# Kernel tuning notes

Hardware: AMD Instinct MI355X
Metric: run time of the kernel (lower is better)

## Reference

```python
import jax, jax.numpy as jnp
import numpy as np

B, T, N, H = 256, 512, 128, 128  # batch, timesteps(l), num_classes, num_hidden


def setup_inputs() -> dict:
    key = jax.random.key(0)
    ks = jax.random.split(key, 7)
    s = 0.05
    return {
        "x": jax.random.normal(ks[0], (B, T, N), dtype=jnp.float32),
        "Wf": jax.random.normal(ks[1], (N, 4 * H), dtype=jnp.float32) * s,
        "Uf": jax.random.normal(ks[2], (H, 4 * H), dtype=jnp.float32) * s,
        "bf": jax.random.normal(ks[3], (4 * H,), dtype=jnp.float32) * s,
        "Wb": jax.random.normal(ks[4], (N, 4 * H), dtype=jnp.float32) * s,
        "Ub": jax.random.normal(ks[5], (H, 4 * H), dtype=jnp.float32) * s,
        "bb": jax.random.normal(ks[6], (4 * H,), dtype=jnp.float32) * s,
    }


def _lstm_scan(xs, W, U, b):
    # xs: [T, B, N]; Keras gate order i, f, g(c), o. Zero initial state.
    def step(carry, xt):
        h, c = carry
        z = xt @ W + h @ U + b  # [B, 4H]
        i, f, g, o = jnp.split(z, 4, axis=-1)
        i = jax.nn.sigmoid(i)
        f = jax.nn.sigmoid(f)
        g = jnp.tanh(g)
        o = jax.nn.sigmoid(o)
        c = f * c + i * g
        h = o * jnp.tanh(c)
        return (h, c), h

    h0 = jnp.zeros((xs.shape[1], U.shape[0]), dtype=xs.dtype)
    c0 = jnp.zeros_like(h0)
    _, hs = jax.lax.scan(step, (h0, c0), xs)
    return hs  # [T, B, H]


def reference(x, Wf, Uf, bf, Wb, Ub, bb):
    xs = jnp.transpose(x, (1, 0, 2))  # [T, B, N]
    f_hs = _lstm_scan(xs, Wf, Uf, bf)            # forward over t = 0..T-1
    b_hs = _lstm_scan(xs[::-1], Wb, Ub, bb)      # backward cell over reversed seq
    # Original code stacks concat(f_h_i, b_h_i) at loop index i WITHOUT
    # re-reversing the backward stream, so we concat step-aligned streams.
    out = jnp.concatenate([f_hs, b_hs], axis=-1)  # [T, B, 2H]
    return jnp.transpose(out, (1, 0, 2))  # [B, T, 2H]
```

## Files before the change

### kernel.cpp

```cpp
#include <hip/hip_runtime.h>


typedef short s16x8 __attribute__((ext_vector_type(8)));
typedef float f32x4 __attribute__((ext_vector_type(4)));

#define NT 512
#define LDSROW 264

#define LDS_BARRIER() asm volatile("s_waitcnt lgkmcnt(0)\n\ts_barrier" ::: "memory")

__device__ __forceinline__ unsigned short f2bf(float f) {
  unsigned int u = __float_as_uint(f);
  u += 0x7fffu + ((u >> 16) & 1u);
  return (unsigned short)(u >> 16);
}
__device__ __forceinline__ float sigm(float x) {
  return __builtin_amdgcn_rcpf(1.f + __expf(-x));
}
__device__ __forceinline__ float tanh_(float x) {
  float xc = fminf(fmaxf(x, -12.f), 12.f);
  return 1.f - 2.f * __builtin_amdgcn_rcpf(1.f + __expf(2.f * xc));
}

__global__ void prep_frags(const float* __restrict__ Wf, const float* __restrict__ Uf,
                           const float* __restrict__ Wb, const float* __restrict__ Ub,
                           unsigned short* __restrict__ frag) {
  int idx = blockIdx.x * 256 + threadIdx.x;
  int j    = idx & 7;
  int lane = (idx >> 3) & 63;
  int tile = (idx >> 9) & 7;
  int kc   = (idx >> 12) & 7;
  int gate = (idx >> 15) & 3;
  int dir  = (idx >> 17) & 1;
  const float* M = (kc < 4) ? (dir ? Wb : Wf) : (dir ? Ub : Uf);
  int k   = (kc & 3) * 32 + (lane >> 4) * 8 + j;
  int col = gate * 128 + tile * 16 + (lane & 15);
  frag[idx] = f2bf(M[k * 512 + col]);
}

__global__ __launch_bounds__(512, 2) void bilstm_rec(
    const unsigned short* __restrict__ frag, const float* __restrict__ x,
    const float* __restrict__ bfw, const float* __restrict__ bbw,
    float* __restrict__ out) {
  __shared__ unsigned short xh[2][16][LDSROW];

  int bid = blockIdx.x;
  int bblk = bid & 63, dir = bid >> 6;
  int tid = threadIdx.x;
  int tc = tid >> 6, lane = tid & 63, quad = lane >> 4, m = lane & 15;
  bool mrow = ((m & 3) == 0);

  s16x8 wu[4][8];
#pragma unroll
  for (int g = 0; g < 4; g++)
#pragma unroll
    for (int kc = 0; kc < 8; kc++)
      wu[g][kc] = *(const s16x8*)(frag +
          ((((size_t)(dir * 4 + g) * 8 + kc) * 8 + tc) * 64 + lane) * 8);

  const float* bias = dir ? bbw : bfw;
  float bv[4];
#pragma unroll
  for (int g = 0; g < 4; g++) bv[g] = bias[g * 128 + tc * 16 + m];

  int srow = tid >> 7, scol = tid & 127;
  const float* xsrc = x + ((size_t)(bblk * 4 + srow) * NT) * 128 + scol;

  auto tmap = [&](int s) { int ss = s > NT - 1 ? NT - 1 : s; return dir ? (NT - 1 - ss) : ss; };

  {
    unsigned int* zp = (unsigned int*)&xh[0][0][0];
    for (int i = tid; i < 2 * 16 * (LDSROW / 2); i += 512) zp[i] = 0;
  }

  float vxA = xsrc[(size_t)tmap(2) * 128];
  float vxB = xsrc[(size_t)tmap(3) * 128];

  float vx1 = xsrc[(size_t)tmap(1) * 128];
  float vx0 = xsrc[(size_t)tmap(0) * 128];
  xh[0][srow * 4][scol] = f2bf(vx1);
  xh[1][srow * 4][scol] = f2bf(vx0);
  __syncthreads();

  s16x8 ah[4], ax[4];
#pragma unroll
  for (int kk = 0; kk < 4; kk++) { ah[kk] = (s16x8){0,0,0,0,0,0,0,0}; ax[kk] = (s16x8){0,0,0,0,0,0,0,0}; }

  if (mrow) {
#pragma unroll
    for (int kk = 0; kk < 4; kk++)
      ax[kk] = *(const s16x8*)(&xh[1][m][kk * 32 + quad * 8]);
  }
  __syncthreads();

  f32x4 accA[4], accB[4];
#pragma unroll
  for (int g = 0; g < 4; g++) {
    accA[g][0] = bv[g]; accA[g][1] = bv[g]; accA[g][2] = bv[g]; accA[g][3] = bv[g];
  }
#pragma unroll
  for (int kk = 0; kk < 4; kk++)
#pragma unroll
    for (int g = 0; g < 4; g++)
      accA[g] = __builtin_amdgcn_mfma_f32_16x16x32_bf16(ax[kk], wu[g][kk], accA[g], 0, 0, 0);

  float cc = 0.f;
  float* outp = out + ((size_t)(bblk * 4 + quad) * NT) * 256 + dir * 128 + tc * 16 + m;

  auto body = [&](int s, float& vx, f32x4 (&accC)[4], f32x4 (&accN)[4]) {
    int cb = s & 1, nb = cb ^ 1;

    float vnew = xsrc[(size_t)tmap(s + 4) * 128];

    if (mrow) {
#pragma unroll
      for (int kk = 0; kk < 4; kk++)
        ah[kk] = *(const s16x8*)(&xh[cb][m][128 + kk * 32 + quad * 8]);
#pragma unroll
      for (int kk = 0; kk < 4; kk++)
        ax[kk] = *(const s16x8*)(&xh[cb][m][kk * 32 + quad * 8]);
    }

#pragma unroll
    for (int kk = 0; kk < 4; kk++)
#pragma unroll
      for (int g = 0; g < 4; g++)
        accC[g] = __builtin_amdgcn_mfma_f32_16x16x32_bf16(ah[kk], wu[g][4 + kk], accC[g], 0, 0, 0);

#pragma unroll
    for (int g = 0; g < 4; g++) {
      accN[g][0] = bv[g]; accN[g][1] = bv[g]; accN[g][2] = bv[g]; accN[g][3] = bv[g];
    }
#pragma unroll
    for (int kk = 0; kk < 4; kk++)
#pragma unroll
      for (int g = 0; g < 4; g++)
        accN[g] = __builtin_amdgcn_mfma_f32_16x16x32_bf16(ax[kk], wu[g][kk], accN[g], 0, 0, 0);

    float iv = sigm(accC[0][0]);
    float fv = sigm(accC[1][0]);
    float gv = tanh_(accC[2][0]);
    float ov = sigm(accC[3][0]);
    cc = fv * cc + iv * gv;
    float hv = ov * tanh_(cc);

    xh[nb][quad * 4][128 + tc * 16 + m] = f2bf(hv);
    xh[nb][srow * 4][scol] = f2bf(vx);

    outp[(size_t)s * 256] = hv;

    LDS_BARRIER();
    vx = vnew;
  };

  for (int s = 0; s < NT; s += 2) {
    body(s, vxA, accA, accB);
    body(s + 1, vxB, accB, accA);
  }
}

extern "C" void kernel_launch(void* const* d_in, const int* in_sizes, int n_in,
                              void* d_out, int out_size, void* d_ws, size_t ws_size,
                              hipStream_t stream) {
  const float* x  = (const float*)d_in[0];
  const float* Wf = (const float*)d_in[1];
  const float* Uf = (const float*)d_in[2];
  const float* bf = (const float*)d_in[3];
  const float* Wb = (const float*)d_in[4];
  const float* Ub = (const float*)d_in[5];
  const float* bb = (const float*)d_in[6];
  float* out = (float*)d_out;

  unsigned short* frag = (unsigned short*)d_ws;

  prep_frags<<<1024, 256, 0, stream>>>(Wf, Uf, Wb, Ub, frag);
  bilstm_rec<<<128, 512, 0, stream>>>(frag, x, bf, bb, out);
}
```

Measured before the change: 473.0 us.

## Batch input projection over four timesteps using full MFMA rows

The input projection x@W is now computed for four timesteps at once by packing four timesteps of x into the sixteen MFMA rows, which were previously mostly zero padding. The result is spread across the four recurrent substeps, and each substep seeds its recurrent accumulator from the matching row. x is loaded as float4 once per four-step group and stored packed as bf16, and h and x now live in separate LDS buffers. This is meant to cut the per-step x MFMA work and global load count, at the cost of more complex pipelining and extra register pressure.

```diff
diff --git a/kernel.cpp b/kernel.cpp
--- a/kernel.cpp
+++ b/kernel.cpp
@@ -5,7 +5,7 @@
 typedef float f32x4 __attribute__((ext_vector_type(4)));
 
 #define NT 512
-#define LDSROW 264
+#define NG 128
 
 #define LDS_BARRIER() asm volatile("s_waitcnt lgkmcnt(0)\n\ts_barrier" ::: "memory")
 
@@ -13,6 +13,9 @@
   unsigned int u = __float_as_uint(f);
   u += 0x7fffu + ((u >> 16) & 1u);
   return (unsigned short)(u >> 16);
+}
+__device__ __forceinline__ unsigned int packbf2(float a, float b) {
+  return (unsigned int)f2bf(a) | ((unsigned int)f2bf(b) << 16);
 }
 __device__ __forceinline__ float sigm(float x) {
   return __builtin_amdgcn_rcpf(1.f + __expf(-x));
@@ -42,7 +45,8 @@
     const unsigned short* __restrict__ frag, const float* __restrict__ x,
     const float* __restrict__ bfw, const float* __restrict__ bbw,
     float* __restrict__ out) {
-  __shared__ unsigned short xh[2][16][LDSROW];
+  __shared__ unsigned short hbuf[2][16][136];
+  __shared__ unsigned short xbuf[2][16][136];
 
   int bid = blockIdx.x;
   int bblk = bid & 63, dir = bid >> 6;
@@ -63,99 +67,114 @@
 #pragma unroll
   for (int g = 0; g < 4; g++) bv[g] = bias[g * 128 + tc * 16 + m];
 
-  int srow = tid >> 7, scol = tid & 127;
-  const float* xsrc = x + ((size_t)(bblk * 4 + srow) * NT) * 128 + scol;
+  int xrow = tid >> 5, xcol = (tid & 31) * 4;
+  int sbr = xrow >> 2, sts = xrow & 3;
+  const float* xsrc = x + ((size_t)(bblk * 4 + sbr) * NT) * 128 + xcol;
 
   auto tmap = [&](int s) { int ss = s > NT - 1 ? NT - 1 : s; return dir ? (NT - 1 - ss) : ss; };
+  auto ldx4 = [&](int G) -> float4 {
+    return *(const float4*)(xsrc + (size_t)tmap(4 * G + sts) * 128);
+  };
+  auto stx = [&](int p, float4 v) {
+    uint2 pk; pk.x = packbf2(v.x, v.y); pk.y = packbf2(v.z, v.w);
+    *(uint2*)(&xbuf[p][xrow][xcol]) = pk;
+  };
 
   {
-    unsigned int* zp = (unsigned int*)&xh[0][0][0];
-    for (int i = tid; i < 2 * 16 * (LDSROW / 2); i += 512) zp[i] = 0;
+    unsigned int* zp = (unsigned int*)&hbuf[0][0][0];
+    for (int i = tid; i < 2 * 16 * 68; i += 512) zp[i] = 0;
   }
-
-  float vxA = xsrc[(size_t)tmap(2) * 128];
-  float vxB = xsrc[(size_t)tmap(3) * 128];
-
-  float vx1 = xsrc[(size_t)tmap(1) * 128];
-  float vx0 = xsrc[(size_t)tmap(0) * 128];
-  xh[0][srow * 4][scol] = f2bf(vx1);
-  xh[1][srow * 4][scol] = f2bf(vx0);
+  stx(0, ldx4(0));
+  stx(1, ldx4(1));
   __syncthreads();
 
-  s16x8 ah[4], ax[4];
+  s16x8 ax[4];
 #pragma unroll
-  for (int kk = 0; kk < 4; kk++) { ah[kk] = (s16x8){0,0,0,0,0,0,0,0}; ax[kk] = (s16x8){0,0,0,0,0,0,0,0}; }
-
-  if (mrow) {
-#pragma unroll
-    for (int kk = 0; kk < 4; kk++)
-      ax[kk] = *(const s16x8*)(&xh[1][m][kk * 32 + quad * 8]);
-  }
-  __syncthreads();
-
-  f32x4 accA[4], accB[4];
+  for (int kk = 0; kk < 4; kk++)
+    ax[kk] = *(const s16x8*)(&xbuf[0][m][kk * 32 + quad * 8]);
+  f32x4 accX0[4], accX1[4];
 #pragma unroll
   for (int g = 0; g < 4; g++) {
-    accA[g][0] = bv[g]; accA[g][1] = bv[g]; accA[g][2] = bv[g]; accA[g][3] = bv[g];
+    accX0[g][0] = bv[g]; accX0[g][1] = bv[g]; accX0[g][2] = bv[g]; accX0[g][3] = bv[g];
   }
 #pragma unroll
   for (int kk = 0; kk < 4; kk++)
 #pragma unroll
     for (int g = 0; g < 4; g++)
-      accA[g] = __builtin_amdgcn_mfma_f32_16x16x32_bf16(ax[kk], wu[g][kk], accA[g], 0, 0, 0);
+      accX0[g] = __builtin_amdgcn_mfma_f32_16x16x32_bf16(ax[kk], wu[g][kk], accX0[g], 0, 0, 0);
+
+  float4 vslot = ldx4(2);
+
+  s16x8 ah[4];
+#pragma unroll
+  for (int kk = 0; kk < 4; kk++) ah[kk] = (s16x8){0, 0, 0, 0, 0, 0, 0, 0};
 
   float cc = 0.f;
   float* outp = out + ((size_t)(bblk * 4 + quad) * NT) * 256 + dir * 128 + tc * 16 + m;
 
-  auto body = [&](int s, float& vx, f32x4 (&accC)[4], f32x4 (&accN)[4]) {
+  auto substep = [&](int s, int sub, int p, f32x4 (&accXc)[4], f32x4 (&accXn)[4]) {
     int cb = s & 1, nb = cb ^ 1;
-
-    float vnew = xsrc[(size_t)tmap(s + 4) * 128];
 
     if (mrow) {
 #pragma unroll
       for (int kk = 0; kk < 4; kk++)
-        ah[kk] = *(const s16x8*)(&xh[cb][m][128 + kk * 32 + quad * 8]);
+        ah[kk] = *(const s16x8*)(&hbuf[cb][m][kk * 32 + quad * 8]);
+    }
+    if (sub == 0) {
 #pragma unroll
       for (int kk = 0; kk < 4; kk++)
-        ax[kk] = *(const s16x8*)(&xh[cb][m][kk * 32 + quad * 8]);
+        ax[kk] = *(const s16x8*)(&xbuf[p ^ 1][m][kk * 32 + quad * 8]);
+#pragma unroll
+      for (int g = 0; g < 4; g++) {
+        accXn[g][0] = bv[g]; accXn[g][1] = bv[g]; accXn[g][2] = bv[g]; accXn[g][3] = bv[g];
+      }
     }
 
-#pragma unroll
-    for (int kk = 0; kk < 4; kk++)
-#pragma unroll
-      for (int g = 0; g < 4; g++)
-        accC[g] = __builtin_amdgcn_mfma_f32_16x16x32_bf16(ah[kk], wu[g][4 + kk], accC[g], 0, 0, 0);
-
+    f32x4 acc[4];
 #pragma unroll
     for (int g = 0; g < 4; g++) {
-      accN[g][0] = bv[g]; accN[g][1] = bv[g]; accN[g][2] = bv[g]; accN[g][3] = bv[g];
+      float z = accXc[g][sub];
+      acc[g][0] = z; acc[g][1] = z; acc[g][2] = z; acc[g][3] = z;
     }
 #pragma unroll
     for (int kk = 0; kk < 4; kk++)
 #pragma unroll
       for (int g = 0; g < 4; g++)
-        accN[g] = __builtin_amdgcn_mfma_f32_16x16x32_bf16(ax[kk], wu[g][kk], accN[g], 0, 0, 0);
+        acc[g] = __builtin_amdgcn_mfma_f32_16x16x32_bf16(ah[kk], wu[g][4 + kk], acc[g], 0, 0, 0);
 
-    float iv = sigm(accC[0][0]);
-    float fv = sigm(accC[1][0]);
-    float gv = tanh_(accC[2][0]);
-    float ov = sigm(accC[3][0]);
+#pragma unroll
+    for (int g = 0; g < 4; g++)
+      accXn[g] = __builtin_amdgcn_mfma_f32_16x16x32_bf16(ax[sub], wu[g][sub], accXn[g], 0, 0, 0);
+
+    float iv = sigm(acc[0][0]);
+    float fv = sigm(acc[1][0]);
+    float gv = tanh_(acc[2][0]);
+    float ov = sigm(acc[3][0]);
     cc = fv * cc + iv * gv;
     float hv = ov * tanh_(cc);
 
-    xh[nb][quad * 4][128 + tc * 16 + m] = f2bf(hv);
-    xh[nb][srow * 4][scol] = f2bf(vx);
-
+    hbuf[nb][quad * 4][tc * 16 + m] = f2bf(hv);
     outp[(size_t)s * 256] = hv;
-
-    LDS_BARRIER();
-    vx = vnew;
   };
 
-  for (int s = 0; s < NT; s += 2) {
-    body(s, vxA, accA, accB);
-    body(s + 1, vxB, accB, accA);
+  auto group = [&](int G, int p, f32x4 (&accXc)[4], f32x4 (&accXn)[4]) {
+    int s0 = 4 * G;
+    float4 vnew = ldx4(G + 3);
+    substep(s0 + 0, 0, p, accXc, accXn);
+    LDS_BARRIER();
+    substep(s0 + 1, 1, p, accXc, accXn);
+    LDS_BARRIER();
+    substep(s0 + 2, 2, p, accXc, accXn);
+    LDS_BARRIER();
+    substep(s0 + 3, 3, p, accXc, accXn);
+    stx(p, vslot);
+    LDS_BARRIER();
+    vslot = vnew;
+  };
+
+  for (int G = 0; G < NG; G += 2) {
+    group(G, 0, accX0, accX1);
+    group(G + 1, 1, accX1, accX0);
   }
 }
 
```

Result: faster. 451.0 us (-4.7%).
